# Performance work log

Hardware: AMD Instinct MI355X
Metric: run time of the kernel (lower is better)

Reference implementation:

```python
import jax, jax.numpy as jnp
import numpy as np

K = 3; STRIDE = 1; PAD = 1
IN_C = 256; OUT_C = 512
SPAN = K * K * IN_C        # 2304, im2col row count
M = 3                      # ALSH augmentation dims
TABLE_SIZE = 8             # hash buckets
R = 2.5                    # LSH bin width


def setup_inputs() -> dict:
    key = jax.random.key(0)
    k1, k2, k3, k4 = jax.random.split(key, 4)
    stdv = 1.0 / np.sqrt(SPAN)
    inp = jax.random.normal(k1, (16, IN_C, 56, 56), dtype=jnp.float32)
    kernels = jax.random.uniform(k2, (OUT_C, SPAN), minval=-stdv, maxval=stdv,
                                 dtype=jnp.float32)
    a_hash = jax.random.normal(k3, (SPAN + M,), dtype=jnp.float32)
    b_hash = jax.random.uniform(k4, (1,), dtype=jnp.float32) * R
    return {"input": inp, "kernels": kernels, "a_hash": a_hash,
            "b_hash": b_hash, "mode": 1}


def _P(x, m):
    # ALSH P-augmentation: append ||x||^(2^i), i=1..m, per row. x: [O, SPAN]
    n = jnp.linalg.norm(x, axis=1, keepdims=True)
    ext = jnp.concatenate([n ** (2 ** (i + 1)) for i in range(m)], axis=1)
    return jnp.concatenate([x, ext], axis=1)  # [O, SPAN+M]


def _bucket(vals, b, r, ts):
    # floor((v+b)/r) ; fmod ts ; abs  (matches torch fmod-then-abs semantics)
    idx = jnp.floor((vals + b) / r).astype(jnp.int32)
    return jnp.abs(jnp.fmod(idx, ts))


def _im2col_matr(x):
    # [N, C, H, W] -> [SPAN, N*H2*W2]
    n = x.shape[0]
    h2 = (x.shape[2] - K + 2 * PAD) // STRIDE + 1
    w2 = (x.shape[3] - K + 2 * PAD) // STRIDE + 1
    patches = jax.lax.conv_general_dilated_patches(
        x, (K, K), (STRIDE, STRIDE), [(PAD, PAD), (PAD, PAD)])  # [N, SPAN, H2, W2]
    return patches.reshape(n, SPAN, h2 * w2).transpose(1, 0, 2).reshape(SPAN, -1), h2, w2


def reference(input, kernels, a_hash, b_hash, mode):
    n = input.shape[0]
    patch_matr, h2, w2 = _im2col_matr(input)  # [SPAN, L]

    # ---- build ALSH table: bucket of each kernel row ----
    kvals = _P(kernels, M) @ a_hash           # [OUT_C]
    kbuck = _bucket(kvals, b_hash[0], R, TABLE_SIZE)

    # ---- vote: hash every unit-normalized patch column, take modal bucket ----
    unit = patch_matr / jnp.linalg.norm(patch_matr, axis=0, keepdims=True)
    q_ext = jnp.full((M, unit.shape[1]), 0.5, dtype=unit.dtype)
    votes = a_hash @ jnp.concatenate([unit, q_ext], axis=0)  # [L]
    vbuck = _bucket(votes, b_hash[0], R, TABLE_SIZE)
    counts = jnp.bincount(vbuck, length=TABLE_SIZE)
    bucket = int(jnp.argmax(counts))

    # ---- gather active kernel rows for that bucket (data-dependent) ----
    rows = np.sort(np.where(np.asarray(kbuck) == bucket)[0])
    if rows.size != 0:
        active = kernels[jnp.asarray(rows)]          # [oc, SPAN]
        out = active @ patch_matr                    # [oc, L]
        if mode:
            out = out / (float(rows.size) / OUT_C)
        oc = int(rows.size)
    else:
        out = kernels @ patch_matr
        oc = OUT_C

    out = out.reshape(oc, n, h2 * w2).transpose(1, 0, 2).reshape(n, oc, h2, w2)
    return (out, jnp.asarray(rows, dtype=jnp.int32))
```

## Files before the change

### kernel.cpp

```cpp
#include <hip/hip_runtime.h>
#include <math.h>

#define N_    16
#define C_    256
#define H_    56
#define W_    56
#define HW_   3136
#define NPIX  50176
#define OUTC  512
#define SPAN_ 2304
#define BLKPX 256
#define HBYTES 24576
#define PXB   128
#define NPB   (NPIX / PXB)

typedef unsigned short u16;
typedef unsigned int   u32;
typedef __attribute__((ext_vector_type(8))) short bf16x8;
typedef __attribute__((ext_vector_type(8))) unsigned short u16x8;
typedef __attribute__((ext_vector_type(4))) float f32x4;
typedef __attribute__((ext_vector_type(4))) unsigned short u16x4;

__device__ __forceinline__ u16 f2bf(float v) {
    u32 x = __float_as_uint(v);
    u32 r = (x + 0x7fffu + ((x >> 16) & 1u)) >> 16;
    return (u16)r;
}

__device__ __forceinline__ int bucketf(float v, float b) {
    int idx = (int)floorf((v + b) / 2.5f);
    int r = idx % 8;
    return r < 0 ? -r : r;
}

__global__ __launch_bounds__(128) void prep2(const float* __restrict__ x,
                                             const float* __restrict__ ah,
                                             const float* __restrict__ bh,
                                             const float* __restrict__ kern,
                                             u16* __restrict__ xp,
                                             float* __restrict__ g,
                                             float* __restrict__ s2,
                                             int* __restrict__ kbuck,
                                             int* __restrict__ counts) {
    int kb = blockIdx.x - NPB;
    int t = threadIdx.x;
    if (kb >= 0) {
        if (kb == 0 && t < 8) counts[t] = 0;
        int oc_l = t >> 1, part = t & 1;
        int oc = kb * 64 + oc_l;
        const float* kr = kern + (size_t)oc * SPAN_ + part * 1152;
        const float* ap = ah + part * 1152;
        float dot = 0.f, ss = 0.f;
        for (int i = 0; i < 288; ++i) {
            float4 kv = *(const float4*)(kr + i * 4);
            float4 av = *(const float4*)(ap + i * 4);
            dot += kv.x * av.x + kv.y * av.y + kv.z * av.z + kv.w * av.w;
            ss  += kv.x * kv.x + kv.y * kv.y + kv.z * kv.z + kv.w * kv.w;
        }
        dot += __shfl_xor(dot, 1);
        ss  += __shfl_xor(ss, 1);
        if (part == 0) {
            float n2 = ss;
            float n4 = n2 * n2;
            float n8 = n4 * n4;
            float v = dot + n2 * ah[SPAN_] + n4 * ah[SPAN_ + 1] +
                      n8 * ah[SPAN_ + 2];
            kbuck[oc] = bucketf(v, bh[0]);
        }
        return;
    }

    __shared__ float aL[SPAN_];
    __shared__ u16 tl[PXB][68];
    for (int j = t; j < SPAN_; j += 128) aL[j] = ah[j];

    const int px = blockIdx.x * PXB + t;
    const int img = px / HW_;
    const size_t xbase = (size_t)img * C_ * HW_ + (px - img * HW_);

    float pg[9];
#pragma unroll
    for (int kk = 0; kk < 9; ++kk) pg[kk] = 0.f;
    float ps = 0.f;
    __syncthreads();

    for (int ph = 0; ph < 4; ++ph) {
        float R[16], Rn[16];
#pragma unroll
        for (int i = 0; i < 16; ++i)
            R[i] = x[xbase + (size_t)(ph * 64 + i) * HW_];
#pragma unroll
        for (int sub = 0; sub < 4; ++sub) {
            if (sub < 3) {
#pragma unroll
                for (int i = 0; i < 16; ++i)
                    Rn[i] = x[xbase + (size_t)(ph * 64 + (sub + 1) * 16 + i) * HW_];
            }
#pragma unroll
            for (int i = 0; i < 16; ++i) {
                int c = ph * 64 + sub * 16 + i;
                float v = R[i];
                const float* ac = &aL[c * 9];
#pragma unroll
                for (int kk = 0; kk < 9; ++kk) pg[kk] += ac[kk] * v;
                ps += v * v;
                tl[t][sub * 16 + i] = f2bf(v);
            }
            if (sub < 3) {
#pragma unroll
                for (int i = 0; i < 16; ++i) R[i] = Rn[i];
            }
        }
        __syncthreads();
        const int oct = t & 7;
#pragma unroll
        for (int pass = 0; pass < 8; ++pass) {
            int pxl = pass * 16 + (t >> 3);
            u16x8 v8 = *(const u16x8*)&tl[pxl][oct * 8];
            *(u16x8*)&xp[((size_t)(blockIdx.x * PXB + pxl)) * C_ +
                         ph * 64 + oct * 8] = v8;
        }
        __syncthreads();
    }

#pragma unroll
    for (int kk = 0; kk < 9; ++kk) g[(size_t)kk * NPIX + px] = pg[kk];
    s2[px] = ps;
}

__global__ __launch_bounds__(256) void vote_kernel(const float* __restrict__ g,
                                                   const float* __restrict__ s2,
                                                   const float* __restrict__ ah,
                                                   const float* __restrict__ bh,
                                                   int* __restrict__ counts) {
    __shared__ int hist[8];
    if (threadIdx.x < 8) hist[threadIdx.x] = 0;
    __syncthreads();
    int q = blockIdx.x * 256 + threadIdx.x;
    int n = q / HW_;
    int p = q - n * HW_;
    int h = p / W_;
    int w = p - h * W_;
    float dot = 0.f, ss = 0.f;
#pragma unroll
    for (int kk = 0; kk < 9; ++kk) {
        int dh = kk / 3 - 1, dw = kk % 3 - 1;
        int hh = h + dh, ww = w + dw;
        if (hh >= 0 && hh < H_ && ww >= 0 && ww < W_) {
            int idx = n * HW_ + hh * W_ + ww;
            dot += g[(size_t)kk * NPIX + idx];
            ss  += s2[idx];
        }
    }
    float qext = 0.5f * (ah[SPAN_] + ah[SPAN_ + 1] + ah[SPAN_ + 2]);
    float v = dot / sqrtf(ss) + qext;
    int b = bucketf(v, bh[0]);
    atomicAdd(&hist[b], 1);
    __syncthreads();
    if (threadIdx.x < 8) atomicAdd(&counts[threadIdx.x], hist[threadIdx.x]);
}

__global__ __launch_bounds__(256) void prep_w(const float* __restrict__ kern,
                                              const int* __restrict__ kbuck,
                                              const int* __restrict__ counts,
                                              const int* __restrict__ mode,
                                              float* __restrict__ out,
                                              u16* __restrict__ wfrag,
                                              int nfB, int oc_total) {
    __shared__ int sc[256];
    __shared__ int rowsL[512];
    int t = threadIdx.x;
    int best = 0, bc = counts[0];
#pragma unroll
    for (int i = 1; i < 8; ++i) {
        int c = counts[i];
        if (c > bc) { bc = c; best = i; }
    }
    int f0 = (kbuck[t] == best) ? 1 : 0;
    int f1 = (kbuck[t + 256] == best) ? 1 : 0;
    sc[t] = f0 | (f1 << 16);
    __syncthreads();
    for (int off = 1; off < 256; off <<= 1) {
        int add = (t >= off) ? sc[t - off] : 0;
        __syncthreads();
        sc[t] += add;
        __syncthreads();
    }
    int tot = sc[255];
    int t0  = tot & 0xffff;
    int cnt = t0 + (tot >> 16);
    int pos0 = (sc[t] & 0xffff) - f0;
    int pos1 = t0 + (sc[t] >> 16) - f1;
    rowsL[t] = 0; rowsL[t + 256] = 0;
    __syncthreads();
    if (cnt == 0) { rowsL[t] = t; rowsL[t + 256] = t + 256; }
    else {
        if (f0) rowsL[pos0] = t;
        if (f1) rowsL[pos1] = t + 256;
    }
    __syncthreads();
    int ocEff = (cnt == 0) ? OUTC : cnt;
    float scale = (mode[0] && cnt > 0) ? 512.0f / (float)cnt : 1.0f;

    if (blockIdx.x == 0) {
        float* rout = out + (size_t)N_ * oc_total * HW_;
        int nw = ocEff < oc_total ? ocEff : oc_total;
        if (cnt == 0) {
            if (t < nw) rout[t] = (float)t;
            if (t + 256 < nw) rout[t + 256] = (float)(t + 256);
        } else {
            if (f0 && pos0 < nw) rout[pos0] = (float)t;
            if (f1 && pos1 < nw) rout[pos1] = (float)(t + 256);
        }
    }

    int e = blockIdx.x * 256 + t;
    int lane = e & 63;
    int t2 = e >> 6;
    int g = t2 % nfB;
    int s = t2 / nfB;
    int kk = s >> 3;
    int cb = s & 7;
    int q = lane >> 4;
    int mcol = lane & 15;
    int oc_i = g * 16 + mcol;
    bool valid = oc_i < ocEff;
    int row = valid ? rowsL[oc_i] : 0;
    const float* kr = kern + (size_t)row * SPAN_;
    u16 w8[8];
#pragma unroll
    for (int j = 0; j < 8; ++j) {
        int c = cb * 32 + q * 8 + j;
        float v = valid ? kr[c * 9 + kk] * scale : 0.f;
        w8[j] = f2bf(v);
    }
    u16* dst = wfrag + ((size_t)((s * nfB + g) * 64 + lane)) * 8;
#pragma unroll
    for (int j = 0; j < 8; ++j) dst[j] = w8[j];
}

__global__ __launch_bounds__(256, 2) void conv_mfma(const u16* __restrict__ xp,
                                                    const u16* __restrict__ wfrag,
                                                    float* __restrict__ out,
                                                    int nfB, int oc_total, int nby) {
    __shared__ char halo[2 * HBYTES];

    int flat = blockIdx.x;
    int bx, by;
    int full = 192 * nby;
    if (flat < full) {
        int gsz = 8 * nby;
        int gi = flat / gsz;
        int tr = flat - gi * gsz;
        by = tr >> 3;
        bx = gi * 8 + (tr & 7);
    } else {
        int tr = flat - full;
        by = tr >> 2;
        bx = 192 + (tr & 3);
    }

    const int t = threadIdx.x;
    const int lane = t & 63;
    const int wv = t >> 6;
    const int pb = bx * BLKPX;
    const int fb = by * 3;
    const int lane15 = lane & 15;
    const int laneq  = lane >> 4;

    u32 valMask[4];
    int aB[4][3];
#pragma unroll
    for (int f = 0; f < 4; ++f) {
        int p = pb + wv * 64 + f * 16 + lane15;
        int img = p / HW_;
        int rp = p - img * HW_;
        int h = rp / W_;
        int w = rp - h * W_;
        u32 m = 0;
#pragma unroll
        for (int kk = 0; kk < 9; ++kk) {
            int dh = kk / 3 - 1, dw = kk % 3 - 1;
            int hh = h + dh, ww = w + dw;
            if (hh >= 0 && hh < H_ && ww >= 0 && ww < W_) m |= (1u << kk);
        }
        valMask[f] = m;
#pragma unroll
        for (int j = 0; j < 3; ++j) {
            int sn = 57 + wv * 64 + f * 16 + lane15 + (j - 1);
            aB[f][j] = sn * 64 + ((laneq ^ ((sn >> 1) & 3)) << 4) - 3584;
        }
    }

    f32x4 acc[4][3];
#pragma unroll
    for (int f = 0; f < 4; ++f)
#pragma unroll
        for (int gg = 0; gg < 3; ++gg) acc[f][gg] = (f32x4){0.f, 0.f, 0.f, 0.f};
    const bf16x8 zf = {0, 0, 0, 0, 0, 0, 0, 0};

    const char* xpb = (const char*)xp;
    const int q4 = (((t & 3) ^ ((t >> 3) & 3)) << 4);
    int gpx[6];
#pragma unroll
    for (int r = 0; r < 6; ++r) {
        int p = pb - 57 + r * 64 + (t >> 2);
        gpx[r] = p < 0 ? 0 : (p >= NPIX ? NPIX - 1 : p);
    }

#pragma unroll
    for (int r = 0; r < 6; ++r)
        __builtin_amdgcn_global_load_lds(
            (const __attribute__((address_space(1))) unsigned int*)
                (xpb + (size_t)gpx[r] * 512 + q4),
            (__attribute__((address_space(3))) unsigned int*)&halo[r * 4096 + t * 16],
            16, 0, 0);

    const size_t cbStride = (size_t)nfB * 512;
    const size_t kkStride = cbStride * 8;
    const u16* wl = wfrag + (size_t)fb * 512 + (size_t)lane * 8;
    bf16x8 bW[3], bWn[3];
#define LOADB(dst, cb_, kk_) do {                                               \
    const u16* _wp = wl + (size_t)(kk_) * kkStride + (size_t)(cb_) * cbStride;  \
    _Pragma("unroll")                                                           \
    for (int _g = 0; _g < 3; ++_g)                                              \
        dst[_g] = *(const bf16x8*)(_wp + (size_t)_g * 512);                     \
} while (0)

    LOADB(bW, 0, 0);

#pragma unroll
    for (int cb = 0; cb < 8; ++cb) {
        __syncthreads();

        if (cb < 7) {
            const int nb = ((cb + 1) & 1) * HBYTES;
#pragma unroll
            for (int r = 0; r < 6; ++r)
                __builtin_amdgcn_global_load_lds(
                    (const __attribute__((address_space(1))) unsigned int*)
                        (xpb + (size_t)gpx[r] * 512 + (cb + 1) * 64 + q4),
                    (__attribute__((address_space(3))) unsigned int*)
                        &halo[nb + r * 4096 + t * 16],
                    16, 0, 0);
        }

#pragma unroll
        for (int kk = 0; kk < 9; ++kk) {
            if (kk < 8)       LOADB(bWn, cb, kk + 1);
            else if (cb < 7)  LOADB(bWn, cb + 1, 0);

            const int dh = kk / 3 - 1;
            const int j  = kk % 3;
            const int IMM = (cb & 1) * HBYTES + (dh + 1) * 3584;
            bf16x8 aX[4];
#pragma unroll
            for (int f = 0; f < 4; ++f) {
                bf16x8 a = *(const bf16x8*)&halo[aB[f][j] + IMM];
                aX[f] = ((valMask[f] >> kk) & 1) ? a : zf;
            }
#pragma unroll
            for (int gg = 0; gg < 3; ++gg)
#pragma unroll
                for (int f = 0; f < 4; ++f)
                    acc[f][gg] = __builtin_amdgcn_mfma_f32_16x16x32_bf16(
                        aX[f], bW[gg], acc[f][gg], 0, 0, 0);
            if (kk < 8 || cb < 7) {
#pragma unroll
                for (int gg = 0; gg < 3; ++gg) bW[gg] = bWn[gg];
            }
        }
    }
#undef LOADB

#pragma unroll
    for (int f = 0; f < 4; ++f) {
        int p0 = pb + wv * 64 + f * 16 + laneq * 4;
        int img0 = p0 / HW_;
        int hw0 = p0 - img0 * HW_;
#pragma unroll
        for (int gg = 0; gg < 3; ++gg) {
            int oc = (fb + gg) * 16 + lane15;
            if (oc < oc_total) {
                float* op = out + ((size_t)img0 * oc_total + oc) * HW_ + hw0;
                *(f32x4*)op = acc[f][gg];
            }
        }
    }
}

extern "C" void kernel_launch(void* const* d_in, const int* in_sizes, int n_in,
                              void* d_out, int out_size, void* d_ws, size_t ws_size,
                              hipStream_t stream) {
    const float* x    = (const float*)d_in[0];
    const float* kern = (const float*)d_in[1];
    const float* ah   = (const float*)d_in[2];
    const float* bh   = (const float*)d_in[3];
    const int*   mode = (const int*)d_in[4];
    float* out = (float*)d_out;

    int oc_total = (out_size % (N_ * HW_ + 1) == 0) ? out_size / (N_ * HW_ + 1)
                                                    : OUTC;
    int nfTot = (oc_total + 15) / 16;
    int nby   = (nfTot + 2) / 3;
    int nfB   = nby * 3;

    u16*   xp     = (u16*)d_ws;
    u16*   wfrag  = xp + (size_t)NPIX * C_;
    float* g      = (float*)(wfrag + (size_t)72 * 36 * 64 * 8);
    float* s2     = g + (size_t)9 * NPIX;
    int*   counts = (int*)(s2 + NPIX);
    int*   kbuck  = counts + 8;

    prep2<<<NPB + 8, 128, 0, stream>>>(x, ah, bh, kern, xp, g, s2, kbuck,
                                       counts);
    vote_kernel<<<NPIX / 256, 256, 0, stream>>>(g, s2, ah, bh, counts);
    prep_w<<<18 * nfB, 256, 0, stream>>>(kern, kbuck, counts, mode, out, wfrag,
                                         nfB, oc_total);
    conv_mfma<<<(NPIX / BLKPX) * nby, 256, 0, stream>>>(xp, wfrag, out, nfB,
                                                        oc_total, nby);
}
```

Baseline: 93.47 us.

## Move kernel hashing to vote kernel, use zero-slot LDS addressing and triple-buffered weights

Moves the per-kernel-row hash computation out of prep2 into extra blocks of vote_kernel, using one wavefront per output channel with shuffle reductions, and zeroes the counts buffer with a memset. In the MFMA conv kernel, out-of-bounds taps are redirected to a zeroed LDS slot via precomputed per-tap addresses, which removes the per-fragment select. Weight fragments are triple-buffered two taps ahead instead of double-buffered, hiding more global load latency at the cost of extra registers. The last halo row load is skipped for four threads so their slot can hold the zero data.

```diff
diff --git a/kernel.cpp b/kernel.cpp
--- a/kernel.cpp
+++ b/kernel.cpp
@@ -11,15 +11,17 @@
 #define SPAN_ 2304
 #define BLKPX 256
 #define HBYTES 24576
+#define ZSLOT 24512
 #define PXB   128
 #define NPB   (NPIX / PXB)
+#define NVB   (NPIX / 256)
 
 typedef unsigned short u16;
 typedef unsigned int   u32;
 typedef __attribute__((ext_vector_type(8))) short bf16x8;
 typedef __attribute__((ext_vector_type(8))) unsigned short u16x8;
+typedef __attribute__((ext_vector_type(4))) unsigned short u16x4;
 typedef __attribute__((ext_vector_type(4))) float f32x4;
-typedef __attribute__((ext_vector_type(4))) unsigned short u16x4;
 
 __device__ __forceinline__ u16 f2bf(float v) {
     u32 x = __float_as_uint(v);
@@ -35,31 +37,94 @@
 
 __global__ __launch_bounds__(128) void prep2(const float* __restrict__ x,
                                              const float* __restrict__ ah,
-                                             const float* __restrict__ bh,
-                                             const float* __restrict__ kern,
                                              u16* __restrict__ xp,
                                              float* __restrict__ g,
-                                             float* __restrict__ s2,
-                                             int* __restrict__ kbuck,
-                                             int* __restrict__ counts) {
-    int kb = blockIdx.x - NPB;
+                                             float* __restrict__ s2) {
     int t = threadIdx.x;
+    __shared__ float aL[SPAN_];
+    __shared__ u16 tl[PXB][68];
+    for (int j = t; j < SPAN_; j += 128) aL[j] = ah[j];
+
+    const int px = blockIdx.x * PXB + t;
+    const int img = px / HW_;
+    const size_t xbase = (size_t)img * C_ * HW_ + (px - img * HW_);
+
+    float pg[9];
+#pragma unroll
+    for (int kk = 0; kk < 9; ++kk) pg[kk] = 0.f;
+    float ps = 0.f;
+    __syncthreads();
+
+    for (int ph = 0; ph < 4; ++ph) {
+        float R[16], Rn[16];
+#pragma unroll
+        for (int i = 0; i < 16; ++i)
+            R[i] = x[xbase + (size_t)(ph * 64 + i) * HW_];
+#pragma unroll
+        for (int sub = 0; sub < 4; ++sub) {
+            if (sub < 3) {
+#pragma unroll
+                for (int i = 0; i < 16; ++i)
+                    Rn[i] = x[xbase + (size_t)(ph * 64 + (sub + 1) * 16 + i) * HW_];
+            }
+#pragma unroll
+            for (int i = 0; i < 16; ++i) {
+                int c = ph * 64 + sub * 16 + i;
+                float v = R[i];
+                const float* ac = &aL[c * 9];
+#pragma unroll
+                for (int kk = 0; kk < 9; ++kk) pg[kk] += ac[kk] * v;
+                ps += v * v;
+                tl[t][sub * 16 + i] = f2bf(v);
+            }
+            if (sub < 3) {
+#pragma unroll
+                for (int i = 0; i < 16; ++i) R[i] = Rn[i];
+            }
+        }
+        __syncthreads();
+        const int oct = t & 7;
+#pragma unroll
+        for (int pass = 0; pass < 8; ++pass) {
+            int pxl = pass * 16 + (t >> 3);
+            u16x8 v8 = *(const u16x8*)&tl[pxl][oct * 8];
+            *(u16x8*)&xp[((size_t)(blockIdx.x * PXB + pxl)) * C_ +
+                         ph * 64 + oct * 8] = v8;
+        }
+        __syncthreads();
+    }
+
+#pragma unroll
+    for (int kk = 0; kk < 9; ++kk) g[(size_t)kk * NPIX + px] = pg[kk];
+    s2[px] = ps;
+}
+
+__global__ __launch_bounds__(256) void vote_kernel(const float* __restrict__ g,
+                                                   const float* __restrict__ s2,
+                                                   const float* __restrict__ ah,
+                                                   const float* __restrict__ bh,
+                                                   const float* __restrict__ kern,
+                                                   int* __restrict__ counts,
+                                                   int* __restrict__ kbuck) {
+    int kb = blockIdx.x - NVB;
     if (kb >= 0) {
-        if (kb == 0 && t < 8) counts[t] = 0;
-        int oc_l = t >> 1, part = t & 1;
-        int oc = kb * 64 + oc_l;
-        const float* kr = kern + (size_t)oc * SPAN_ + part * 1152;
-        const float* ap = ah + part * 1152;
+        int wv = threadIdx.x >> 6, lane = threadIdx.x & 63;
+        int oc = kb * 4 + wv;
+        const float* kr = kern + (size_t)oc * SPAN_;
         float dot = 0.f, ss = 0.f;
-        for (int i = 0; i < 288; ++i) {
-            float4 kv = *(const float4*)(kr + i * 4);
-            float4 av = *(const float4*)(ap + i * 4);
+#pragma unroll
+        for (int i = 0; i < 9; ++i) {
+            float4 kv = *(const float4*)(kr + i * 256 + lane * 4);
+            float4 av = *(const float4*)(ah + i * 256 + lane * 4);
             dot += kv.x * av.x + kv.y * av.y + kv.z * av.z + kv.w * av.w;
             ss  += kv.x * kv.x + kv.y * kv.y + kv.z * kv.z + kv.w * kv.w;
         }
-        dot += __shfl_xor(dot, 1);
-        ss  += __shfl_xor(ss, 1);
-        if (part == 0) {
+#pragma unroll
+        for (int off = 32; off; off >>= 1) {
+            dot += __shfl_xor(dot, off);
+            ss  += __shfl_xor(ss, off);
+        }
+        if (lane == 0) {
             float n2 = ss;
             float n4 = n2 * n2;
             float n8 = n4 * n4;
@@ -70,69 +135,6 @@
         return;
     }
 
-    __shared__ float aL[SPAN_];
-    __shared__ u16 tl[PXB][68];
-    for (int j = t; j < SPAN_; j += 128) aL[j] = ah[j];
-
-    const int px = blockIdx.x * PXB + t;
-    const int img = px / HW_;
-    const size_t xbase = (size_t)img * C_ * HW_ + (px - img * HW_);
-
-    float pg[9];
-#pragma unroll
-    for (int kk = 0; kk < 9; ++kk) pg[kk] = 0.f;
-    float ps = 0.f;
-    __syncthreads();
-
-    for (int ph = 0; ph < 4; ++ph) {
-        float R[16], Rn[16];
-#pragma unroll
-        for (int i = 0; i < 16; ++i)
-            R[i] = x[xbase + (size_t)(ph * 64 + i) * HW_];
-#pragma unroll
-        for (int sub = 0; sub < 4; ++sub) {
-            if (sub < 3) {
-#pragma unroll
-                for (int i = 0; i < 16; ++i)
-                    Rn[i] = x[xbase + (size_t)(ph * 64 + (sub + 1) * 16 + i) * HW_];
-            }
-#pragma unroll
-            for (int i = 0; i < 16; ++i) {
-                int c = ph * 64 + sub * 16 + i;
-                float v = R[i];
-                const float* ac = &aL[c * 9];
-#pragma unroll
-                for (int kk = 0; kk < 9; ++kk) pg[kk] += ac[kk] * v;
-                ps += v * v;
-                tl[t][sub * 16 + i] = f2bf(v);
-            }
-            if (sub < 3) {
-#pragma unroll
-                for (int i = 0; i < 16; ++i) R[i] = Rn[i];
-            }
-        }
-        __syncthreads();
-        const int oct = t & 7;
-#pragma unroll
-        for (int pass = 0; pass < 8; ++pass) {
-            int pxl = pass * 16 + (t >> 3);
-            u16x8 v8 = *(const u16x8*)&tl[pxl][oct * 8];
-            *(u16x8*)&xp[((size_t)(blockIdx.x * PXB + pxl)) * C_ +
-                         ph * 64 + oct * 8] = v8;
-        }
-        __syncthreads();
-    }
-
-#pragma unroll
-    for (int kk = 0; kk < 9; ++kk) g[(size_t)kk * NPIX + px] = pg[kk];
-    s2[px] = ps;
-}
-
-__global__ __launch_bounds__(256) void vote_kernel(const float* __restrict__ g,
-                                                   const float* __restrict__ s2,
-                                                   const float* __restrict__ ah,
-                                                   const float* __restrict__ bh,
-                                                   int* __restrict__ counts) {
     __shared__ int hist[8];
     if (threadIdx.x < 8) hist[threadIdx.x] = 0;
     __syncthreads();
@@ -268,8 +270,12 @@
     const int lane15 = lane & 15;
     const int laneq  = lane >> 4;
 
-    u32 valMask[4];
-    int aB[4][3];
+    if (t < 8) {
+        int off = ((t & 4) ? HBYTES : 0) + ZSLOT + (t & 3) * 16;
+        *(u16x8*)&halo[off] = (u16x8){0, 0, 0, 0, 0, 0, 0, 0};
+    }
+
+    int addrA[4][9];
 #pragma unroll
     for (int f = 0; f < 4; ++f) {
         int p = pb + wv * 64 + f * 16 + lane15;
@@ -277,18 +283,14 @@
         int rp = p - img * HW_;
         int h = rp / W_;
         int w = rp - h * W_;
-        u32 m = 0;
 #pragma unroll
         for (int kk = 0; kk < 9; ++kk) {
             int dh = kk / 3 - 1, dw = kk % 3 - 1;
             int hh = h + dh, ww = w + dw;
-            if (hh >= 0 && hh < H_ && ww >= 0 && ww < W_) m |= (1u << kk);
-        }
-        valMask[f] = m;
-#pragma unroll
-        for (int j = 0; j < 3; ++j) {
-            int sn = 57 + wv * 64 + f * 16 + lane15 + (j - 1);
-            aB[f][j] = sn * 64 + ((laneq ^ ((sn >> 1) & 3)) << 4) - 3584;
+            bool val = (hh >= 0) & (hh < H_) & (ww >= 0) & (ww < W_);
+            int sn = 57 + wv * 64 + f * 16 + lane15 + dw;
+            int base = sn * 64 + ((laneq ^ ((sn >> 1) & 3)) << 4) - 3584;
+            addrA[f][kk] = val ? base : (ZSLOT - (kk / 3) * 3584);
         }
     }
 
@@ -297,7 +299,6 @@
     for (int f = 0; f < 4; ++f)
 #pragma unroll
         for (int gg = 0; gg < 3; ++gg) acc[f][gg] = (f32x4){0.f, 0.f, 0.f, 0.f};
-    const bf16x8 zf = {0, 0, 0, 0, 0, 0, 0, 0};
 
     const char* xpb = (const char*)xp;
     const int q4 = (((t & 3) ^ ((t >> 3) & 3)) << 4);
@@ -309,25 +310,29 @@
     }
 
 #pragma unroll
-    for (int r = 0; r < 6; ++r)
-        __builtin_amdgcn_global_load_lds(
-            (const __attribute__((address_space(1))) unsigned int*)
-                (xpb + (size_t)gpx[r] * 512 + q4),
-            (__attribute__((address_space(3))) unsigned int*)&halo[r * 4096 + t * 16],
-            16, 0, 0);
+    for (int r = 0; r < 6; ++r) {
+        if (r < 5 || t < 252)
+            __builtin_amdgcn_global_load_lds(
+                (const __attribute__((address_space(1))) unsigned int*)
+                    (xpb + (size_t)gpx[r] * 512 + q4),
+                (__attribute__((address_space(3))) unsigned int*)
+                    &halo[r * 4096 + t * 16],
+                16, 0, 0);
+    }
 
     const size_t cbStride = (size_t)nfB * 512;
     const size_t kkStride = cbStride * 8;
     const u16* wl = wfrag + (size_t)fb * 512 + (size_t)lane * 8;
-    bf16x8 bW[3], bWn[3];
-#define LOADB(dst, cb_, kk_) do {                                               \
+    bf16x8 bB[3][3];
+#define LOADB(slot, cb_, kk_) do {                                              \
     const u16* _wp = wl + (size_t)(kk_) * kkStride + (size_t)(cb_) * cbStride;  \
     _Pragma("unroll")                                                           \
     for (int _g = 0; _g < 3; ++_g)                                              \
-        dst[_g] = *(const bf16x8*)(_wp + (size_t)_g * 512);                     \
+        bB[slot][_g] = *(const bf16x8*)(_wp + (size_t)_g * 512);                \
 } while (0)
 
-    LOADB(bW, 0, 0);
+    LOADB(0, 0, 0);
+    LOADB(1, 0, 1);
 
 #pragma unroll
     for (int cb = 0; cb < 8; ++cb) {
@@ -336,39 +341,33 @@
         if (cb < 7) {
             const int nb = ((cb + 1) & 1) * HBYTES;
 #pragma unroll
-            for (int r = 0; r < 6; ++r)
-                __builtin_amdgcn_global_load_lds(
-                    (const __attribute__((address_space(1))) unsigned int*)
-                        (xpb + (size_t)gpx[r] * 512 + (cb + 1) * 64 + q4),
-                    (__attribute__((address_space(3))) unsigned int*)
-                        &halo[nb + r * 4096 + t * 16],
-                    16, 0, 0);
+            for (int r = 0; r < 6; ++r) {
+                if (r < 5 || t < 252)
+                    __builtin_amdgcn_global_load_lds(
+                        (const __attribute__((address_space(1))) unsigned int*)
+                            (xpb + (size_t)gpx[r] * 512 + (cb + 1) * 64 + q4),
+                        (__attribute__((address_space(3))) unsigned int*)
+                            &halo[nb + r * 4096 + t * 16],
+                        16, 0, 0);
+            }
         }
 
 #pragma unroll
         for (int kk = 0; kk < 9; ++kk) {
-            if (kk < 8)       LOADB(bWn, cb, kk + 1);
-            else if (cb < 7)  LOADB(bWn, cb + 1, 0);
-
-            const int dh = kk / 3 - 1;
-            const int j  = kk % 3;
-            const int IMM = (cb & 1) * HBYTES + (dh + 1) * 3584;
+            if (kk < 7)       LOADB((kk + 2) % 3, cb, kk + 2);
+            else if (cb < 7)  LOADB((kk + 2) % 3, cb + 1, kk - 7);
+
+            const int IMM = (cb & 1) * HBYTES + (kk / 3) * 3584;
             bf16x8 aX[4];
 #pragma unroll
-            for (int f = 0; f < 4; ++f) {
-                bf16x8 a = *(const bf16x8*)&halo[aB[f][j] + IMM];
-                aX[f] = ((valMask[f] >> kk) & 1) ? a : zf;
-            }
+            for (int f = 0; f < 4; ++f)
+                aX[f] = *(const bf16x8*)&halo[addrA[f][kk] + IMM];
 #pragma unroll
             for (int gg = 0; gg < 3; ++gg)
 #pragma unroll
                 for (int f = 0; f < 4; ++f)
                     acc[f][gg] = __builtin_amdgcn_mfma_f32_16x16x32_bf16(
-                        aX[f], bW[gg], acc[f][gg], 0, 0, 0);
-            if (kk < 8 || cb < 7) {
-#pragma unroll
-                for (int gg = 0; gg < 3; ++gg) bW[gg] = bWn[gg];
-            }
+                        aX[f], bB[kk % 3][gg], acc[f][gg], 0, 0, 0);
         }
     }
 #undef LOADB
@@ -412,9 +411,11 @@
     int*   counts = (int*)(s2 + NPIX);
     int*   kbuck  = counts + 8;
 
-    prep2<<<NPB + 8, 128, 0, stream>>>(x, ah, bh, kern, xp, g, s2, kbuck,
-                                       counts);
-    vote_kernel<<<NPIX / 256, 256, 0, stream>>>(g, s2, ah, bh, counts);
+    hipMemsetAsync(counts, 0, 8 * sizeof(int), stream);
+
+    prep2<<<NPB, 128, 0, stream>>>(x, ah, xp, g, s2);
+    vote_kernel<<<NVB + 128, 256, 0, stream>>>(g, s2, ah, bh, kern, counts,
+                                               kbuck);
     prep_w<<<18 * nfB, 256, 0, stream>>>(kern, kbuck, counts, mode, out, wfrag,
                                          nfB, oc_total);
     conv_mfma<<<(NPIX / BLKPX) * nby, 256, 0, stream>>>(xp, wfrag, out, nfB,
```

Result: slower. 113.7 us (+21.6%).

## Split input prep across channel halves and move kernel hashing into vote kernel

Applied to the files above, without the earlier changes.

The prep kernel is split so that each 128-pixel tile is handled by two blocks, one per half of the channels. Each block writes partial projection and squared-norm sums, and the vote kernel adds the two halves together. Kernel-row hashing moves from prep into the vote kernel and is rewritten as one wave per output channel with a shuffle reduction. The counts reset becomes a memset, and wfrag now aliases the scratch buffer once the vote kernel has consumed it. The aim is twice as many prep blocks for better occupancy and latency hiding, at the cost of extra partial-sum traffic and reads in the vote kernel.

```diff
diff --git a/kernel.cpp b/kernel.cpp
--- a/kernel.cpp
+++ b/kernel.cpp
@@ -12,14 +12,15 @@
 #define BLKPX 256
 #define HBYTES 24576
 #define PXB   128
-#define NPB   (NPIX / PXB)
+#define NPB2  (2 * NPIX / PXB)
+#define NVB   (NPIX / 256)
 
 typedef unsigned short u16;
 typedef unsigned int   u32;
 typedef __attribute__((ext_vector_type(8))) short bf16x8;
 typedef __attribute__((ext_vector_type(8))) unsigned short u16x8;
+typedef __attribute__((ext_vector_type(4))) unsigned short u16x4;
 typedef __attribute__((ext_vector_type(4))) float f32x4;
-typedef __attribute__((ext_vector_type(4))) unsigned short u16x4;
 
 __device__ __forceinline__ u16 f2bf(float v) {
     u32 x = __float_as_uint(v);
@@ -33,33 +34,102 @@
     return r < 0 ? -r : r;
 }
 
-__global__ __launch_bounds__(128) void prep2(const float* __restrict__ x,
-                                             const float* __restrict__ ah,
-                                             const float* __restrict__ bh,
-                                             const float* __restrict__ kern,
-                                             u16* __restrict__ xp,
-                                             float* __restrict__ g,
-                                             float* __restrict__ s2,
-                                             int* __restrict__ kbuck,
-                                             int* __restrict__ counts) {
-    int kb = blockIdx.x - NPB;
+__global__ __launch_bounds__(128) void prep2h(const float* __restrict__ x,
+                                              const float* __restrict__ ah,
+                                              u16* __restrict__ xp,
+                                              float* __restrict__ gp,
+                                              float* __restrict__ s2p) {
     int t = threadIdx.x;
+    const int half = blockIdx.x & 1;
+    const int tile = blockIdx.x >> 1;
+    const int coff = half * 128;
+
+    __shared__ float aL[128 * 9];
+    __shared__ u16 tl[PXB][68];
+    for (int j = t; j < 128 * 9; j += 128) aL[j] = ah[coff * 9 + j];
+
+    const int px = tile * PXB + t;
+    const int img = px / HW_;
+    const size_t xbase = (size_t)img * C_ * HW_ + (px - img * HW_);
+
+    float pg[9];
+#pragma unroll
+    for (int kk = 0; kk < 9; ++kk) pg[kk] = 0.f;
+    float ps = 0.f;
+    __syncthreads();
+
+    for (int ph = 0; ph < 2; ++ph) {
+        const int c0 = coff + ph * 64;
+        float R[16], Rn[16];
+#pragma unroll
+        for (int i = 0; i < 16; ++i)
+            R[i] = x[xbase + (size_t)(c0 + i) * HW_];
+#pragma unroll
+        for (int sub = 0; sub < 4; ++sub) {
+            if (sub < 3) {
+#pragma unroll
+                for (int i = 0; i < 16; ++i)
+                    Rn[i] = x[xbase + (size_t)(c0 + (sub + 1) * 16 + i) * HW_];
+            }
+#pragma unroll
+            for (int i = 0; i < 16; ++i) {
+                int cl = ph * 64 + sub * 16 + i;
+                float v = R[i];
+                const float* ac = &aL[cl * 9];
+#pragma unroll
+                for (int kk = 0; kk < 9; ++kk) pg[kk] += ac[kk] * v;
+                ps += v * v;
+                tl[t][sub * 16 + i] = f2bf(v);
+            }
+            if (sub < 3) {
+#pragma unroll
+                for (int i = 0; i < 16; ++i) R[i] = Rn[i];
+            }
+        }
+        __syncthreads();
+        const int oct = t & 7;
+#pragma unroll
+        for (int pass = 0; pass < 8; ++pass) {
+            int pxl = pass * 16 + (t >> 3);
+            u16x8 v8 = *(const u16x8*)&tl[pxl][oct * 8];
+            *(u16x8*)&xp[((size_t)(tile * PXB + pxl)) * C_ +
+                         c0 + oct * 8] = v8;
+        }
+        __syncthreads();
+    }
+
+    float* gh = gp + (size_t)half * 9 * NPIX;
+#pragma unroll
+    for (int kk = 0; kk < 9; ++kk) gh[(size_t)kk * NPIX + px] = pg[kk];
+    s2p[(size_t)half * NPIX + px] = ps;
+}
+
+__global__ __launch_bounds__(256) void vote_kernel(const float* __restrict__ gp,
+                                                   const float* __restrict__ s2p,
+                                                   const float* __restrict__ ah,
+                                                   const float* __restrict__ bh,
+                                                   const float* __restrict__ kern,
+                                                   int* __restrict__ counts,
+                                                   int* __restrict__ kbuck) {
+    int kb = blockIdx.x - NVB;
     if (kb >= 0) {
-        if (kb == 0 && t < 8) counts[t] = 0;
-        int oc_l = t >> 1, part = t & 1;
-        int oc = kb * 64 + oc_l;
-        const float* kr = kern + (size_t)oc * SPAN_ + part * 1152;
-        const float* ap = ah + part * 1152;
+        int wv = threadIdx.x >> 6, lane = threadIdx.x & 63;
+        int oc = kb * 4 + wv;
+        const float* kr = kern + (size_t)oc * SPAN_;
         float dot = 0.f, ss = 0.f;
-        for (int i = 0; i < 288; ++i) {
-            float4 kv = *(const float4*)(kr + i * 4);
-            float4 av = *(const float4*)(ap + i * 4);
+#pragma unroll
+        for (int i = 0; i < 9; ++i) {
+            float4 kv = *(const float4*)(kr + i * 256 + lane * 4);
+            float4 av = *(const float4*)(ah + i * 256 + lane * 4);
             dot += kv.x * av.x + kv.y * av.y + kv.z * av.z + kv.w * av.w;
             ss  += kv.x * kv.x + kv.y * kv.y + kv.z * kv.z + kv.w * kv.w;
         }
-        dot += __shfl_xor(dot, 1);
-        ss  += __shfl_xor(ss, 1);
-        if (part == 0) {
+#pragma unroll
+        for (int off = 32; off; off >>= 1) {
+            dot += __shfl_xor(dot, off);
+            ss  += __shfl_xor(ss, off);
+        }
+        if (lane == 0) {
             float n2 = ss;
             float n4 = n2 * n2;
             float n8 = n4 * n4;
@@ -70,69 +140,6 @@
         return;
     }
 
-    __shared__ float aL[SPAN_];
-    __shared__ u16 tl[PXB][68];
-    for (int j = t; j < SPAN_; j += 128) aL[j] = ah[j];
-
-    const int px = blockIdx.x * PXB + t;
-    const int img = px / HW_;
-    const size_t xbase = (size_t)img * C_ * HW_ + (px - img * HW_);
-
-    float pg[9];
-#pragma unroll
-    for (int kk = 0; kk < 9; ++kk) pg[kk] = 0.f;
-    float ps = 0.f;
-    __syncthreads();
-
-    for (int ph = 0; ph < 4; ++ph) {
-        float R[16], Rn[16];
-#pragma unroll
-        for (int i = 0; i < 16; ++i)
-            R[i] = x[xbase + (size_t)(ph * 64 + i) * HW_];
-#pragma unroll
-        for (int sub = 0; sub < 4; ++sub) {
-            if (sub < 3) {
-#pragma unroll
-                for (int i = 0; i < 16; ++i)
-                    Rn[i] = x[xbase + (size_t)(ph * 64 + (sub + 1) * 16 + i) * HW_];
-            }
-#pragma unroll
-            for (int i = 0; i < 16; ++i) {
-                int c = ph * 64 + sub * 16 + i;
-                float v = R[i];
-                const float* ac = &aL[c * 9];
-#pragma unroll
-                for (int kk = 0; kk < 9; ++kk) pg[kk] += ac[kk] * v;
-                ps += v * v;
-                tl[t][sub * 16 + i] = f2bf(v);
-            }
-            if (sub < 3) {
-#pragma unroll
-                for (int i = 0; i < 16; ++i) R[i] = Rn[i];
-            }
-        }
-        __syncthreads();
-        const int oct = t & 7;
-#pragma unroll
-        for (int pass = 0; pass < 8; ++pass) {
-            int pxl = pass * 16 + (t >> 3);
-            u16x8 v8 = *(const u16x8*)&tl[pxl][oct * 8];
-            *(u16x8*)&xp[((size_t)(blockIdx.x * PXB + pxl)) * C_ +
-                         ph * 64 + oct * 8] = v8;
-        }
-        __syncthreads();
-    }
-
-#pragma unroll
-    for (int kk = 0; kk < 9; ++kk) g[(size_t)kk * NPIX + px] = pg[kk];
-    s2[px] = ps;
-}
-
-__global__ __launch_bounds__(256) void vote_kernel(const float* __restrict__ g,
-                                                   const float* __restrict__ s2,
-                                                   const float* __restrict__ ah,
-                                                   const float* __restrict__ bh,
-                                                   int* __restrict__ counts) {
     __shared__ int hist[8];
     if (threadIdx.x < 8) hist[threadIdx.x] = 0;
     __syncthreads();
@@ -141,6 +148,8 @@
     int p = q - n * HW_;
     int h = p / W_;
     int w = p - h * W_;
+    const float* g0 = gp;
+    const float* g1 = gp + (size_t)9 * NPIX;
     float dot = 0.f, ss = 0.f;
 #pragma unroll
     for (int kk = 0; kk < 9; ++kk) {
@@ -148,8 +157,8 @@
         int hh = h + dh, ww = w + dw;
         if (hh >= 0 && hh < H_ && ww >= 0 && ww < W_) {
             int idx = n * HW_ + hh * W_ + ww;
-            dot += g[(size_t)kk * NPIX + idx];
-            ss  += s2[idx];
+            dot += g0[(size_t)kk * NPIX + idx] + g1[(size_t)kk * NPIX + idx];
+            ss  += s2p[idx] + s2p[(size_t)NPIX + idx];
         }
     }
     float qext = 0.5f * (ah[SPAN_] + ah[SPAN_ + 1] + ah[SPAN_ + 2]);
@@ -406,15 +415,18 @@
     int nfB   = nby * 3;
 
     u16*   xp     = (u16*)d_ws;
-    u16*   wfrag  = xp + (size_t)NPIX * C_;
-    float* g      = (float*)(wfrag + (size_t)72 * 36 * 64 * 8);
-    float* s2     = g + (size_t)9 * NPIX;
-    int*   counts = (int*)(s2 + NPIX);
+    float* scratch = (float*)(xp + (size_t)NPIX * C_);
+    float* gp     = scratch;
+    float* s2p    = scratch + (size_t)18 * NPIX;
+    u16*   wfrag  = (u16*)scratch;
+    int*   counts = (int*)(scratch + (size_t)20 * NPIX);
     int*   kbuck  = counts + 8;
 
-    prep2<<<NPB + 8, 128, 0, stream>>>(x, ah, bh, kern, xp, g, s2, kbuck,
-                                       counts);
-    vote_kernel<<<NPIX / 256, 256, 0, stream>>>(g, s2, ah, bh, counts);
+    hipMemsetAsync(counts, 0, 8 * sizeof(int), stream);
+
+    prep2h<<<NPB2, 128, 0, stream>>>(x, ah, xp, gp, s2p);
+    vote_kernel<<<NVB + 128, 256, 0, stream>>>(gp, s2p, ah, bh, kern, counts,
+                                               kbuck);
     prep_w<<<18 * nfB, 256, 0, stream>>>(kern, kbuck, counts, mode, out, wfrag,
                                          nfB, oc_total);
     conv_mfma<<<(NPIX / BLKPX) * nby, 256, 0, stream>>>(xp, wfrag, out, nfB,
```

After: 91.12 us. 2.5% less time.
